# Kernel optimization log

Measured on AMD Instinct MI355X. Metric: run time of the kernel, lower is better.

Reference implementation:

```python
import jax, jax.numpy as jnp
import numpy as np

B, T, DIM, H, DH = 4, 4096, 1024, 16, 64


def setup_inputs() -> dict:
    key = jax.random.key(0)
    ks = jax.random.split(key, 6)
    s = lambda fan_in: 1.0 / np.sqrt(fan_in)
    x = jax.random.normal(ks[0], (B, T, DIM), dtype=jnp.float32)
    Wq = jax.random.uniform(ks[1], (DIM, H * DH), jnp.float32, -s(DIM), s(DIM))
    Wk = jax.random.uniform(ks[2], (DIM, H * DH), jnp.float32, -s(DIM), s(DIM))
    Wv = jax.random.uniform(ks[3], (DIM, H * DH), jnp.float32, -s(DIM), s(DIM))
    Wo = jax.random.uniform(ks[4], (H * DH, DIM), jnp.float32, -s(H * DH), s(H * DH))
    bo = jax.random.uniform(ks[5], (DIM,), jnp.float32, -s(H * DH), s(H * DH))
    return {"x": x, "Wq": Wq, "Wk": Wk, "Wv": Wv, "Wo": Wo, "bo": bo}


def reference(x, Wq, Wk, Wv, Wo, bo):
    b, t, _ = x.shape
    # projections (no bias, matching nn.Linear(bias=False))
    to_heads = lambda y: y.reshape(b, t, H, DH).transpose(0, 2, 1, 3)  # bhnd
    q = to_heads(x @ Wq)
    k = to_heads(x @ Wk)
    v = to_heads(x @ Wv)
    # linear attention: softmax over feature dim for q, over seq dim for k
    q = jax.nn.softmax(q, axis=-1) * (DH ** -0.5)
    k = jax.nn.softmax(k, axis=-2)
    context = jnp.einsum('bhnd,bhne->bhde', k, v)   # [b,h,dh,dh]
    attn = jnp.einsum('bhnd,bhde->bhne', q, context)  # [b,h,n,dh]
    attn = attn.transpose(0, 2, 1, 3).reshape(b, t, H * DH)
    return attn @ Wo + bo  # dropout is identity at p=0.0 / eval
```

## Files before the change

kernel.cpp:

```cpp
#include <hip/hip_runtime.h>
#include <hip/hip_bf16.h>
#include <cstdint>
#include <cstddef>

#define BB 4
#define TT 4096
#define HH 16
#define NROWS 16384

typedef __attribute__((ext_vector_type(8))) short bf16x8;
typedef __attribute__((ext_vector_type(4))) float f32x4;

__device__ __forceinline__ void gload_lds16(const void* g, void* l) {
  __builtin_amdgcn_global_load_lds(
      (const __attribute__((address_space(1))) void*)g,
      (__attribute__((address_space(3))) void*)l, 16, 0, 0);
}

template <int N>
__device__ __forceinline__ void wait_vmcnt() {
  if constexpr (N == 4)
    asm volatile("s_waitcnt vmcnt(4)" ::: "memory");
  else
    asm volatile("s_waitcnt vmcnt(0)" ::: "memory");
  __builtin_amdgcn_sched_barrier(0);
}

__device__ __forceinline__ void hbar() {
  asm volatile("s_barrier" ::: "memory");
  __builtin_amdgcn_sched_barrier(0);
}

__global__ __launch_bounds__(256) void xconv_k(const float* __restrict__ x,
                                               __hip_bfloat16* __restrict__ xb) {
  const size_t i = ((size_t)blockIdx.x * 256 + threadIdx.x) * 8;
  float4 a = *(const float4*)&x[i];
  float4 b = *(const float4*)&x[i + 4];
  __hip_bfloat16 o[8] __attribute__((aligned(16)));
  o[0] = __float2bfloat16(a.x); o[1] = __float2bfloat16(a.y);
  o[2] = __float2bfloat16(a.z); o[3] = __float2bfloat16(a.w);
  o[4] = __float2bfloat16(b.x); o[5] = __float2bfloat16(b.y);
  o[6] = __float2bfloat16(b.z); o[7] = __float2bfloat16(b.w);
  *(int4*)&xb[i] = *(const int4*)o;
}

__global__ __launch_bounds__(256) void wconv_k(const float* __restrict__ Wq,
                                               const float* __restrict__ Wk,
                                               const float* __restrict__ Wv,
                                               const float* __restrict__ Wo,
                                               __hip_bfloat16* __restrict__ WT) {
  const int which = blockIdx.z;
  const float* W = which == 0 ? Wq : which == 1 ? Wk : which == 2 ? Wv : Wo;
  __shared__ float tile[64][65];
  const int n0 = blockIdx.x * 64, k0 = blockIdx.y * 64;
  const int t = threadIdx.x;
  const int r = t >> 2;
  const int cq = (t & 3) * 16;
#pragma unroll
  for (int i = 0; i < 4; ++i) {
    float4 v = *(const float4*)&W[(size_t)(k0 + r) * 1024 + n0 + cq + i * 4];
    tile[r][cq + i * 4 + 0] = v.x;
    tile[r][cq + i * 4 + 1] = v.y;
    tile[r][cq + i * 4 + 2] = v.z;
    tile[r][cq + i * 4 + 3] = v.w;
  }
  __syncthreads();
  __hip_bfloat16 ob[16] __attribute__((aligned(16)));
#pragma unroll
  for (int j = 0; j < 16; ++j) ob[j] = __float2bfloat16(tile[cq + j][r]);
  __hip_bfloat16* dst = WT + (size_t)(which * 1024 + n0 + r) * 1024 + k0 + cq;
  *(int4*)dst = *(const int4*)&ob[0];
  *(int4*)(dst + 8) = *(const int4*)&ob[8];
}

template <int OMODE, int PB>
__global__ __launch_bounds__(512) void mgemm3_k(
    const __hip_bfloat16* __restrict__ A, int lda,
    const __hip_bfloat16* __restrict__ BT, const float* __restrict__ bias,
    void* __restrict__ Cp, int ldc, int gx) {
  __shared__ __hip_bfloat16 lds[2][32768];

  const int t = threadIdx.x;
  const int wid = t >> 6, l = t & 63;
  const int wr = wid >> 2, wc = wid & 3;

  const int nwg = gridDim.x;
  const int cpx = nwg >> 3;
  const int bid = blockIdx.x;
  const int swz = (bid & 7) * cpx + (bid >> 3);
  const int bx = swz % gx, by = swz / gx;
  const int row0 = by * 256, col0 = bx * 256;

  const __hip_bfloat16* BTb = PB ? BT + ((size_t)(row0 >> 12) << 20) : BT;

  const int sg = l >> 3;
  const int octp = ((l & 7) + sg) & 7;
  const int koct = octp & 3;
  const int srow = 2 * (wid * 16 + sg) + (octp >> 2);
  const __hip_bfloat16* As0 = A + (size_t)(row0 + srow) * lda + koct * 8;
  const __hip_bfloat16* Bs0 = BTb + (size_t)(col0 + srow) * 1024 + koct * 8;

  f32x4 acc[8][4];
#pragma unroll
  for (int m = 0; m < 8; ++m)
#pragma unroll
    for (int n = 0; n < 4; ++n) acc[m][n] = (f32x4){0.f, 0.f, 0.f, 0.f};

  const int lr = l & 15, hk = l >> 4;
  const int slot = (((lr & 1) << 2) + hk - (lr >> 1)) & 7;
  const int rdo = (lr >> 1) * 64 + slot * 8;

  auto stageA = [&](int tn, int c) {
    __hip_bfloat16* d = &lds[tn & 1][c * 8192 + wid * 1024];
    const __hip_bfloat16* s = As0 + tn * 64 + c * 32;
    gload_lds16(s, d);
    gload_lds16(s + (size_t)16 * lda, d + 512);
  };
  auto stageB = [&](int tn, int c) {
    __hip_bfloat16* d = &lds[tn & 1][16384 + c * 8192 + wid * 1024];
    const __hip_bfloat16* s = Bs0 + tn * 64 + c * 32;
    gload_lds16(s, d);
    gload_lds16(s + (size_t)16 * 1024, d + 512);
  };

  stageA(0, 0); stageB(0, 0); stageA(0, 1); stageB(0, 1);

  const __hip_bfloat16* sb = &lds[0][0];
  for (int tn = 0; tn < 16; ++tn) {
    const int bufo = (tn & 1) * 32768;
    const bool pre = tn < 15;
    bf16x8 bfv[4], afv[4];

    wait_vmcnt<4>();
    hbar();
    if (pre) stageA(tn + 1, 0);
#pragma unroll
    for (int n = 0; n < 4; ++n)
      bfv[n] = *(const bf16x8*)(sb + bufo + 16384 + wc * 2048 + n * 512 + rdo);
#pragma unroll
    for (int j = 0; j < 4; ++j)
      afv[j] = *(const bf16x8*)(sb + bufo + wr * 4096 + j * 512 + rdo);
    __builtin_amdgcn_s_setprio(1);
#pragma unroll
    for (int j = 0; j < 4; ++j)
#pragma unroll
      for (int n = 0; n < 4; ++n)
        acc[j][n] = __builtin_amdgcn_mfma_f32_16x16x32_bf16(afv[j], bfv[n],
                                                            acc[j][n], 0, 0, 0);
    __builtin_amdgcn_s_setprio(0);
    if (pre) stageB(tn + 1, 0);
#pragma unroll
    for (int j = 0; j < 4; ++j)
      afv[j] = *(const bf16x8*)(sb + bufo + wr * 4096 + 2048 + j * 512 + rdo);
    __builtin_amdgcn_s_setprio(1);
#pragma unroll
    for (int j = 0; j < 4; ++j)
#pragma unroll
      for (int n = 0; n < 4; ++n)
        acc[4 + j][n] = __builtin_amdgcn_mfma_f32_16x16x32_bf16(
            afv[j], bfv[n], acc[4 + j][n], 0, 0, 0);
    __builtin_amdgcn_s_setprio(0);

    if (pre)
      wait_vmcnt<4>();
    else
      wait_vmcnt<0>();
    hbar();
    if (pre) stageA(tn + 1, 1);
#pragma unroll
    for (int n = 0; n < 4; ++n)
      bfv[n] = *(const bf16x8*)(sb + bufo + 8192 + 16384 + wc * 2048 +
                                n * 512 + rdo);
#pragma unroll
    for (int j = 0; j < 4; ++j)
      afv[j] = *(const bf16x8*)(sb + bufo + 8192 + wr * 4096 + j * 512 + rdo);
    __builtin_amdgcn_s_setprio(1);
#pragma unroll
    for (int j = 0; j < 4; ++j)
#pragma unroll
      for (int n = 0; n < 4; ++n)
        acc[j][n] = __builtin_amdgcn_mfma_f32_16x16x32_bf16(afv[j], bfv[n],
                                                            acc[j][n], 0, 0, 0);
    __builtin_amdgcn_s_setprio(0);
    if (pre) stageB(tn + 1, 1);
#pragma unroll
    for (int j = 0; j < 4; ++j)
      afv[j] = *(const bf16x8*)(sb + bufo + 8192 + wr * 4096 + 2048 + j * 512 +
                                rdo);
    __builtin_amdgcn_s_setprio(1);
#pragma unroll
    for (int j = 0; j < 4; ++j)
#pragma unroll
      for (int n = 0; n < 4; ++n)
        acc[4 + j][n] = __builtin_amdgcn_mfma_f32_16x16x32_bf16(
            afv[j], bfv[n], acc[4 + j][n], 0, 0, 0);
    __builtin_amdgcn_s_setprio(0);
  }

  const int cr = hk * 4;
  const int cc = lr;
  if constexpr (OMODE == 0) {
    __hip_bfloat16* C = (__hip_bfloat16*)Cp;
#pragma unroll
    for (int m = 0; m < 8; ++m)
#pragma unroll
      for (int n = 0; n < 4; ++n) {
        const size_t cb = (size_t)(row0 + wr * 128 + m * 16 + cr) * ldc +
                          col0 + wc * 64 + n * 16 + cc;
#pragma unroll
        for (int j = 0; j < 4; ++j)
          C[cb + (size_t)j * ldc] = __float2bfloat16(acc[m][n][j]);
      }
  } else {
    float* C = (float*)Cp;
    float bv[4];
#pragma unroll
    for (int n = 0; n < 4; ++n) bv[n] = bias[col0 + wc * 64 + n * 16 + cc];
#pragma unroll
    for (int m = 0; m < 8; ++m)
#pragma unroll
      for (int n = 0; n < 4; ++n) {
        const size_t cb = (size_t)(row0 + wr * 128 + m * 16 + cr) * ldc +
                          col0 + wc * 64 + n * 16 + cc;
#pragma unroll
        for (int j = 0; j < 4; ++j)
          C[cb + (size_t)j * ldc] = acc[m][n][j] + bv[n];
      }
  }
}

__global__ __launch_bounds__(256) void ctx_partial_k(
    const __hip_bfloat16* __restrict__ qkv, float* __restrict__ part,
    float* __restrict__ den) {
  const int bh = blockIdx.x;
  const int s = blockIdx.y;
  const int b = bh >> 4;
  const int h = bh & 15;
  const int n0 = s * 128;

  __shared__ float ek[128][64];
  __shared__ float vf[128][64];

  const int t = threadIdx.x;
  const int rr = t >> 1;
  const int c0 = (t & 1) * 32;
  const size_t base = (size_t)(b * TT + n0 + rr) * 3072 + 1024 + h * 64 + c0;
#pragma unroll
  for (int i = 0; i < 4; ++i) {
    int4 kq = *(const int4*)(qkv + base + i * 8);
    int4 vq = *(const int4*)(qkv + base + 1024 + i * 8);
    const __hip_bfloat16* kp = (const __hip_bfloat16*)&kq;
    const __hip_bfloat16* vp = (const __hip_bfloat16*)&vq;
#pragma unroll
    for (int j = 0; j < 8; ++j) {
      ek[rr][c0 + i * 8 + j] = __expf(__bfloat162float(kp[j]));
      vf[rr][c0 + i * 8 + j] = __bfloat162float(vp[j]);
    }
  }
  __syncthreads();

  const int lane = t & 63, w = t >> 6;
  const int dblk = (lane & 7) | ((w & 1) << 3);
  const int eblk = (lane >> 3) | ((w >> 1) << 3);
  const int d0 = dblk * 4, e0 = eblk * 4;

  float acc[4][4];
#pragma unroll
  for (int i = 0; i < 4; ++i)
#pragma unroll
    for (int j = 0; j < 4; ++j) acc[i][j] = 0.f;

  for (int n = 0; n < 128; ++n) {
    float4 ekv = *(const float4*)&ek[n][d0];
    float4 vv = *(const float4*)&vf[n][e0];
    acc[0][0] += ekv.x * vv.x; acc[0][1] += ekv.x * vv.y;
    acc[0][2] += ekv.x * vv.z; acc[0][3] += ekv.x * vv.w;
    acc[1][0] += ekv.y * vv.x; acc[1][1] += ekv.y * vv.y;
    acc[1][2] += ekv.y * vv.z; acc[1][3] += ekv.y * vv.w;
    acc[2][0] += ekv.z * vv.x; acc[2][1] += ekv.z * vv.y;
    acc[2][2] += ekv.z * vv.z; acc[2][3] += ekv.z * vv.w;
    acc[3][0] += ekv.w * vv.x; acc[3][1] += ekv.w * vv.y;
    acc[3][2] += ekv.w * vv.z; acc[3][3] += ekv.w * vv.w;
  }

  float* pb = part + ((size_t)bh * 32 + s) * 4096;
#pragma unroll
  for (int di = 0; di < 4; ++di) {
    float4 o = {acc[di][0], acc[di][1], acc[di][2], acc[di][3]};
    *(float4*)&pb[(d0 + di) * 64 + e0] = o;
  }

  if (t < 64) {
    float sden = 0.0f;
    for (int n = 0; n < 128; ++n) sden += ek[n][t];
    den[((size_t)bh * 32 + s) * 64 + t] = sden;
  }
}

__global__ __launch_bounds__(256) void ctx_reduce_k(
    const float* __restrict__ part, const float* __restrict__ den,
    __hip_bfloat16* __restrict__ ctxb) {
  const int bh = blockIdx.x, q = blockIdx.y, t = threadIdx.x;
  const int idx = q * 1024 + t * 4;
  const int d = idx >> 6;
  float sden = 0.f;
  for (int s = 0; s < 32; ++s) sden += den[((size_t)bh * 32 + s) * 64 + d];
  float4 sv = {0.f, 0.f, 0.f, 0.f};
  const float* pb = part + (size_t)bh * 32 * 4096 + idx;
  for (int s = 0; s < 32; ++s) {
    float4 v = *(const float4*)(pb + (size_t)s * 4096);
    sv.x += v.x; sv.y += v.y; sv.z += v.z; sv.w += v.w;
  }
  const float di = 1.0f / sden;
  __hip_bfloat16 ob[4] __attribute__((aligned(8)));
  ob[0] = __float2bfloat16(sv.x * di);
  ob[1] = __float2bfloat16(sv.y * di);
  ob[2] = __float2bfloat16(sv.z * di);
  ob[3] = __float2bfloat16(sv.w * di);
  *(int2*)&ctxb[(size_t)bh * 4096 + idx] = *(const int2*)ob;
}

__global__ __launch_bounds__(256) void qsm_k(__hip_bfloat16* __restrict__ qkv) {
  const int t = threadIdx.x;
  const int w = t >> 6, l = t & 63;
  const int n0 = blockIdx.x * 8;
#pragma unroll
  for (int i = 0; i < 4; ++i) {
    const int u = i * 4 + w;
    const int row = n0 + (u >> 1);
    const int half = u & 1;
    __hip_bfloat16* p = qkv + (size_t)row * 3072 + half * 512 + l * 8;
    int4 raw = *(const int4*)p;
    const __hip_bfloat16* bp = (const __hip_bfloat16*)&raw;
    float v[8];
    float m = -1e30f;
#pragma unroll
    for (int j = 0; j < 8; ++j) {
      v[j] = __bfloat162float(bp[j]);
      m = fmaxf(m, v[j]);
    }
    m = fmaxf(m, __shfl_xor(m, 1));
    m = fmaxf(m, __shfl_xor(m, 2));
    m = fmaxf(m, __shfl_xor(m, 4));
    float s = 0.f;
#pragma unroll
    for (int j = 0; j < 8; ++j) {
      v[j] = __expf(v[j] - m);
      s += v[j];
    }
    s += __shfl_xor(s, 1);
    s += __shfl_xor(s, 2);
    s += __shfl_xor(s, 4);
    const float inv = 0.125f / s;
    __hip_bfloat16 o[8] __attribute__((aligned(16)));
#pragma unroll
    for (int j = 0; j < 8; ++j) o[j] = __float2bfloat16(v[j] * inv);
    *(int4*)p = *(const int4*)o;
  }
}

__global__ __launch_bounds__(256) void wfuse_k(
    const __hip_bfloat16* __restrict__ WT,
    const __hip_bfloat16* __restrict__ ctxb, __hip_bfloat16* __restrict__ WfT) {
  const int bh = blockIdx.x;
  const int b = bh >> 4, h = bh & 15;
  const int t = threadIdx.x, w = t >> 6, l = t & 63;
  const int n1 = blockIdx.y * 64 + w * 16;
  const int lr = l & 15, hk = l >> 4;

  f32x4 acc[4];
#pragma unroll
  for (int n = 0; n < 4; ++n) acc[n] = (f32x4){0.f, 0.f, 0.f, 0.f};

  const __hip_bfloat16* Abase =
      WT + (size_t)(3072 + n1 + lr) * 1024 + h * 64 + hk * 8;
  const __hip_bfloat16* Bbase = ctxb + (size_t)bh * 4096 + hk * 8;

#pragma unroll
  for (int kk2 = 0; kk2 < 2; ++kk2) {
    bf16x8 af = *(const bf16x8*)(Abase + kk2 * 32);
#pragma unroll
    for (int n = 0; n < 4; ++n) {
      bf16x8 bf = *(const bf16x8*)(Bbase + (n * 16 + lr) * 64 + kk2 * 32);
      acc[n] = __builtin_amdgcn_mfma_f32_16x16x32_bf16(af, bf, acc[n], 0, 0, 0);
    }
  }

  __hip_bfloat16* W0 = WfT + ((size_t)b << 20) + (size_t)(n1 + hk * 4) * 1024 +
                       h * 64 + lr;
#pragma unroll
  for (int n = 0; n < 4; ++n)
#pragma unroll
    for (int j = 0; j < 4; ++j)
      W0[(size_t)j * 1024 + n * 16] = __float2bfloat16(acc[n][j]);
}

extern "C" void kernel_launch(void* const* d_in, const int* in_sizes, int n_in,
                              void* d_out, int out_size, void* d_ws,
                              size_t ws_size, hipStream_t stream) {
  const float* x = (const float*)d_in[0];
  const float* Wq = (const float*)d_in[1];
  const float* Wk = (const float*)d_in[2];
  const float* Wv = (const float*)d_in[3];
  const float* Wo = (const float*)d_in[4];
  const float* bo = (const float*)d_in[5];
  float* out = (float*)d_out;

  char* ws = (char*)d_ws;
  __hip_bfloat16* qkv = (__hip_bfloat16*)ws;
  __hip_bfloat16* WT = (__hip_bfloat16*)(ws + 100663296ull);
  float* den = (float*)(ws + 100663296ull + 8388608ull);
  __hip_bfloat16* ctxb =
      (__hip_bfloat16*)(ws + 100663296ull + 8388608ull + 524288ull);
  __hip_bfloat16* WfT =
      (__hip_bfloat16*)(ws + 100663296ull + 8388608ull + 1048576ull);
  __hip_bfloat16* xb = (__hip_bfloat16*)d_out;
  float* part = (float*)((char*)d_out + 33554432ull);

  const dim3 blk(256);

  xconv_k<<<dim3(NROWS * 1024 / 8 / 256), blk, 0, stream>>>(x, xb);
  wconv_k<<<dim3(16, 16, 4), blk, 0, stream>>>(Wq, Wk, Wv, Wo, WT);

  mgemm3_k<0, 0><<<dim3(768), dim3(512), 0, stream>>>(xb, 1024, WT, nullptr,
                                                      qkv, 3072, 12);

  ctx_partial_k<<<dim3(64, 32), blk, 0, stream>>>(qkv, part, den);
  ctx_reduce_k<<<dim3(64, 4), blk, 0, stream>>>(part, den, ctxb);
  qsm_k<<<dim3(2048), blk, 0, stream>>>(qkv);
  wfuse_k<<<dim3(64, 16), blk, 0, stream>>>(WT, ctxb, WfT);

  mgemm3_k<1, 1><<<dim3(256), dim3(512), 0, stream>>>(qkv, 3072, WfT, bo, out,
                                                      1024, 4);
}
```

Baseline: 228.3 us.

## Fuse Q softmax into context kernel and compute K^T V with bf16 MFMA

Removes the separate Q-softmax kernel: each context-partial block now also applies the per-head softmax to its 128-row Q tile in place, which saves one launch and one pass over Q. The K^T V partial product moves from scalar FP32 FMAs over float LDS tiles to bf16 MFMA 16x16x32, with exp(K) and V stored transposed in bf16 LDS using a padded, swizzled layout. This halves the LDS footprint and uses matrix cores. The cost is extra precision loss, since exp(K) is rounded to bf16 before both the product and the denominator sum.

```diff
diff --git a/kernel.cpp b/kernel.cpp
--- a/kernel.cpp
+++ b/kernel.cpp
@@ -229,71 +229,121 @@
   }
 }
 
-__global__ __launch_bounds__(256) void ctx_partial_k(
-    const __hip_bfloat16* __restrict__ qkv, float* __restrict__ part,
-    float* __restrict__ den) {
+__global__ __launch_bounds__(256) void ctxq_k(__hip_bfloat16* __restrict__ qkv,
+                                              float* __restrict__ part,
+                                              float* __restrict__ den) {
+  __shared__ __hip_bfloat16 ldsb[2 * 8736];
+  __hip_bfloat16* ekT = ldsb;
+  __hip_bfloat16* vfT = ldsb + 8736;
+
   const int bh = blockIdx.x;
   const int s = blockIdx.y;
   const int b = bh >> 4;
   const int h = bh & 15;
   const int n0 = s * 128;
-
-  __shared__ float ek[128][64];
-  __shared__ float vf[128][64];
-
   const int t = threadIdx.x;
+
   const int rr = t >> 1;
   const int c0 = (t & 1) * 32;
   const size_t base = (size_t)(b * TT + n0 + rr) * 3072 + 1024 + h * 64 + c0;
+  int4 kq[4], vq[4];
 #pragma unroll
   for (int i = 0; i < 4; ++i) {
-    int4 kq = *(const int4*)(qkv + base + i * 8);
-    int4 vq = *(const int4*)(qkv + base + 1024 + i * 8);
-    const __hip_bfloat16* kp = (const __hip_bfloat16*)&kq;
-    const __hip_bfloat16* vp = (const __hip_bfloat16*)&vq;
+    kq[i] = *(const int4*)(qkv + base + i * 8);
+    vq[i] = *(const int4*)(qkv + base + 1024 + i * 8);
+  }
+
+  {
+    const int g8 = t >> 3;
+    const int lc = (t & 7) * 8;
+#pragma unroll
+    for (int it = 0; it < 4; ++it) {
+      const int r = it * 32 + g8;
+      __hip_bfloat16* p =
+          qkv + (size_t)(b * TT + n0 + r) * 3072 + h * 64 + lc;
+      int4 raw = *(const int4*)p;
+      const __hip_bfloat16* bp = (const __hip_bfloat16*)&raw;
+      float v[8];
+      float m = -1e30f;
+#pragma unroll
+      for (int j = 0; j < 8; ++j) {
+        v[j] = __bfloat162float(bp[j]);
+        m = fmaxf(m, v[j]);
+      }
+      m = fmaxf(m, __shfl_xor(m, 1));
+      m = fmaxf(m, __shfl_xor(m, 2));
+      m = fmaxf(m, __shfl_xor(m, 4));
+      float sm = 0.f;
+#pragma unroll
+      for (int j = 0; j < 8; ++j) {
+        v[j] = __expf(v[j] - m);
+        sm += v[j];
+      }
+      sm += __shfl_xor(sm, 1);
+      sm += __shfl_xor(sm, 2);
+      sm += __shfl_xor(sm, 4);
+      const float inv = 0.125f / sm;
+      __hip_bfloat16 o[8] __attribute__((aligned(16)));
+#pragma unroll
+      for (int j = 0; j < 8; ++j) o[j] = __float2bfloat16(v[j] * inv);
+      *(int4*)p = *(const int4*)o;
+    }
+  }
+
+#pragma unroll
+  for (int i = 0; i < 4; ++i) {
+    const __hip_bfloat16* kp = (const __hip_bfloat16*)&kq[i];
+    const __hip_bfloat16* vp = (const __hip_bfloat16*)&vq[i];
 #pragma unroll
     for (int j = 0; j < 8; ++j) {
-      ek[rr][c0 + i * 8 + j] = __expf(__bfloat162float(kp[j]));
-      vf[rr][c0 + i * 8 + j] = __bfloat162float(vp[j]);
+      const int c = c0 + i * 8 + j;
+      const int off = c * 136 + ((c >> 5) & 1) * 32 + rr;
+      ekT[off] = __float2bfloat16(__expf(__bfloat162float(kp[j])));
+      vfT[off] = vp[j];
     }
   }
   __syncthreads();
 
-  const int lane = t & 63, w = t >> 6;
-  const int dblk = (lane & 7) | ((w & 1) << 3);
-  const int eblk = (lane >> 3) | ((w >> 1) << 3);
-  const int d0 = dblk * 4, e0 = eblk * 4;
-
-  float acc[4][4];
-#pragma unroll
-  for (int i = 0; i < 4; ++i)
-#pragma unroll
-    for (int j = 0; j < 4; ++j) acc[i][j] = 0.f;
-
-  for (int n = 0; n < 128; ++n) {
-    float4 ekv = *(const float4*)&ek[n][d0];
-    float4 vv = *(const float4*)&vf[n][e0];
-    acc[0][0] += ekv.x * vv.x; acc[0][1] += ekv.x * vv.y;
-    acc[0][2] += ekv.x * vv.z; acc[0][3] += ekv.x * vv.w;
-    acc[1][0] += ekv.y * vv.x; acc[1][1] += ekv.y * vv.y;
-    acc[1][2] += ekv.y * vv.z; acc[1][3] += ekv.y * vv.w;
-    acc[2][0] += ekv.z * vv.x; acc[2][1] += ekv.z * vv.y;
-    acc[2][2] += ekv.z * vv.z; acc[2][3] += ekv.z * vv.w;
-    acc[3][0] += ekv.w * vv.x; acc[3][1] += ekv.w * vv.y;
-    acc[3][2] += ekv.w * vv.z; acc[3][3] += ekv.w * vv.w;
+  const int w = t >> 6, l = t & 63;
+  const int lr = l & 15, hk = l >> 4;
+  f32x4 acc[4];
+#pragma unroll
+  for (int n = 0; n < 4; ++n) acc[n] = (f32x4){0.f, 0.f, 0.f, 0.f};
+
+  const int arow = w * 16 + lr;
+  const int abase = arow * 136 + ((arow >> 5) & 1) * 32 + hk * 8;
+#pragma unroll
+  for (int ks = 0; ks < 4; ++ks) {
+    bf16x8 af = *(const bf16x8*)(ekT + abase + ks * 32);
+#pragma unroll
+    for (int n = 0; n < 4; ++n) {
+      const int brow = n * 16 + lr;
+      bf16x8 bf = *(const bf16x8*)(vfT + brow * 136 + ((brow >> 5) & 1) * 32 +
+                                   hk * 8 + ks * 32);
+      acc[n] =
+          __builtin_amdgcn_mfma_f32_16x16x32_bf16(af, bf, acc[n], 0, 0, 0);
+    }
   }
 
   float* pb = part + ((size_t)bh * 32 + s) * 4096;
 #pragma unroll
-  for (int di = 0; di < 4; ++di) {
-    float4 o = {acc[di][0], acc[di][1], acc[di][2], acc[di][3]};
-    *(float4*)&pb[(d0 + di) * 64 + e0] = o;
-  }
-
-  if (t < 64) {
-    float sden = 0.0f;
-    for (int n = 0; n < 128; ++n) sden += ek[n][t];
-    den[((size_t)bh * 32 + s) * 64 + t] = sden;
+  for (int n = 0; n < 4; ++n)
+#pragma unroll
+    for (int j = 0; j < 4; ++j)
+      pb[(w * 16 + hk * 4 + j) * 64 + n * 16 + lr] = acc[n][j];
+
+  if ((t & 3) == 0) {
+    const int d = t >> 2;
+    const int dbase = d * 136 + ((d >> 5) & 1) * 32;
+    float sden = 0.f;
+#pragma unroll
+    for (int q8 = 0; q8 < 16; ++q8) {
+      bf16x8 e8 = *(const bf16x8*)(ekT + dbase + q8 * 8);
+      const __hip_bfloat16* ep = (const __hip_bfloat16*)&e8;
+#pragma unroll
+      for (int j = 0; j < 8; ++j) sden += __bfloat162float(ep[j]);
+    }
+    den[((size_t)bh * 32 + s) * 64 + d] = sden;
   }
 }
 
@@ -320,45 +370,6 @@
   *(int2*)&ctxb[(size_t)bh * 4096 + idx] = *(const int2*)ob;
 }
 
-__global__ __launch_bounds__(256) void qsm_k(__hip_bfloat16* __restrict__ qkv) {
-  const int t = threadIdx.x;
-  const int w = t >> 6, l = t & 63;
-  const int n0 = blockIdx.x * 8;
-#pragma unroll
-  for (int i = 0; i < 4; ++i) {
-    const int u = i * 4 + w;
-    const int row = n0 + (u >> 1);
-    const int half = u & 1;
-    __hip_bfloat16* p = qkv + (size_t)row * 3072 + half * 512 + l * 8;
-    int4 raw = *(const int4*)p;
-    const __hip_bfloat16* bp = (const __hip_bfloat16*)&raw;
-    float v[8];
-    float m = -1e30f;
-#pragma unroll
-    for (int j = 0; j < 8; ++j) {
-      v[j] = __bfloat162float(bp[j]);
-      m = fmaxf(m, v[j]);
-    }
-    m = fmaxf(m, __shfl_xor(m, 1));
-    m = fmaxf(m, __shfl_xor(m, 2));
-    m = fmaxf(m, __shfl_xor(m, 4));
-    float s = 0.f;
-#pragma unroll
-    for (int j = 0; j < 8; ++j) {
-      v[j] = __expf(v[j] - m);
-      s += v[j];
-    }
-    s += __shfl_xor(s, 1);
-    s += __shfl_xor(s, 2);
-    s += __shfl_xor(s, 4);
-    const float inv = 0.125f / s;
-    __hip_bfloat16 o[8] __attribute__((aligned(16)));
-#pragma unroll
-    for (int j = 0; j < 8; ++j) o[j] = __float2bfloat16(v[j] * inv);
-    *(int4*)p = *(const int4*)o;
-  }
-}
-
 __global__ __launch_bounds__(256) void wfuse_k(
     const __hip_bfloat16* __restrict__ WT,
     const __hip_bfloat16* __restrict__ ctxb, __hip_bfloat16* __restrict__ WfT) {
@@ -425,9 +436,8 @@
   mgemm3_k<0, 0><<<dim3(768), dim3(512), 0, stream>>>(xb, 1024, WT, nullptr,
                                                       qkv, 3072, 12);
 
-  ctx_partial_k<<<dim3(64, 32), blk, 0, stream>>>(qkv, part, den);
+  ctxq_k<<<dim3(64, 32), blk, 0, stream>>>(qkv, part, den);
   ctx_reduce_k<<<dim3(64, 4), blk, 0, stream>>>(part, den, ctxb);
-  qsm_k<<<dim3(2048), blk, 0, stream>>>(qkv);
   wfuse_k<<<dim3(64, 16), blk, 0, stream>>>(WT, ctxb, WfT);
 
   mgemm3_k<1, 1><<<dim3(256), dim3(512), 0, stream>>>(qkv, 3072, WfT, bo, out,
```

New measurement: 195.4 us. 1.17x faster.
